# Performance work log

Hardware: AMD Instinct MI355X
Metric: run time of the kernel (lower is better)

## Reference

```python
import jax, jax.numpy as jnp
import numpy as np

N_WINDOW = 128  # |i-j| < N_WINDOW kept
D_K = 64

def setup_inputs() -> dict:
    key = jax.random.key(0)
    kq, kk, kv = jax.random.split(key, 3)
    B, H, S, D = 2, 8, 2048, D_K
    Q = jax.random.normal(kq, (B, H, S, D), dtype=jnp.float32)
    K = jax.random.normal(kk, (B, H, S, D), dtype=jnp.float32)
    V = jax.random.normal(kv, (B, H, S, D), dtype=jnp.float32)
    return {"Q": Q, "K": K, "V": V}

def reference(Q, K, V):
    S = Q.shape[-2]
    # scores: [B, H, S, S]
    scores = jnp.einsum('bhqd,bhkd->bhqk', Q, K) / jnp.sqrt(jnp.float32(D_K))
    idx = jnp.arange(S)
    band = jnp.abs(idx[:, None] - idx[None, :]) < N_WINDOW  # [S, S] band mask
    scores = jnp.where(band[None, None, :, :], scores, -jnp.inf)
    attn = jax.nn.softmax(scores, axis=-1)
    context = jnp.einsum('bhqk,bhkd->bhqd', attn, V)
    return (context, attn)
```

## Files before the change

### kernel.cpp

```cpp
#include <hip/hip_runtime.h>
#include <math.h>

#define S_LEN 2048
#define DK 64
#define NW 128
#define TQ 32
#define CH 32
#define NCH 10
#define KLW 320
#define PSTR 324
#define PSTR4 81
#define SSTR 68
#define SSTR4 17

#define DOT4(acc, a, b) \
    acc.x = fmaf(a.x, b.x, acc.x); \
    acc.y = fmaf(a.y, b.y, acc.y); \
    acc.z = fmaf(a.z, b.z, acc.z); \
    acc.w = fmaf(a.w, b.w, acc.w);

#define AXPY4(acc, s, v) \
    acc.x = fmaf(s, v.x, acc.x); \
    acc.y = fmaf(s, v.y, acc.y); \
    acc.z = fmaf(s, v.z, acc.z); \
    acc.w = fmaf(s, v.w, acc.w);

__global__ __launch_bounds__(256, 2) void band_attn_tile(
    const float* __restrict__ Q,
    const float* __restrict__ K,
    const float* __restrict__ V,
    float* __restrict__ ctx_out,
    float* __restrict__ attn_out)
{
    __shared__ float Qs[TQ * SSTR];
    __shared__ float St[CH * SSTR];
    __shared__ float Ps[TQ * PSTR];

    const int tid  = threadIdx.x;
    const int bh   = blockIdx.x >> 6;
    const int q0   = (blockIdx.x & 63) * TQ;
    const int base = q0 - (NW - 1);

    float4* Qs4 = (float4*)Qs;
    float4* St4 = (float4*)St;
    float4* Ps4 = (float4*)Ps;

    {
        const float4* Q4 = (const float4*)(Q + ((size_t)bh * S_LEN + q0) * DK);
        #pragma unroll
        for (int h = 0; h < 2; ++h) {
            int idx = tid + h * 256;
            int r = idx >> 4, c4 = idx & 15;
            float4 v = Q4[r * 16 + c4];
            v.x *= 0.125f; v.y *= 0.125f; v.z *= 0.125f; v.w *= 0.125f;
            Qs4[r * SSTR4 + c4] = v;
        }
    }

    const int q2 = tid >> 4;
    const int kb = tid & 15;
    const int qA = 2 * q2, qB = qA + 1;

    const float4* Kh4 = (const float4*)(K + (size_t)bh * S_LEN * DK);
    const float4* Vh4 = (const float4*)(V + (size_t)bh * S_LEN * DK);

    for (int c = 0; c < NCH; ++c) {
        __syncthreads();
        #pragma unroll
        for (int h = 0; h < 2; ++h) {
            int idx = tid + h * 256;
            int r = idx >> 4, c4 = idx & 15;
            int kg = base + c * CH + r;
            float4 v = {0.f, 0.f, 0.f, 0.f};
            if (kg >= 0 && kg < S_LEN) v = Kh4[(size_t)kg * 16 + c4];
            St4[r * SSTR4 + c4] = v;
        }
        __syncthreads();

        float4 a00 = {0,0,0,0}, a01 = {0,0,0,0}, a10 = {0,0,0,0}, a11 = {0,0,0,0};
        #pragma unroll
        for (int j = 0; j < 16; ++j) {
            float4 qa = Qs4[qA * SSTR4 + j];
            float4 qb = Qs4[qB * SSTR4 + j];
            float4 k0 = St4[kb * SSTR4 + j];
            float4 k1 = St4[(kb + 16) * SSTR4 + j];
            DOT4(a00, qa, k0); DOT4(a01, qa, k1);
            DOT4(a10, qb, k0); DOT4(a11, qb, k1);
        }
        float s00 = (a00.x + a00.y) + (a00.z + a00.w);
        float s01 = (a01.x + a01.y) + (a01.z + a01.w);
        float s10 = (a10.x + a10.y) + (a10.z + a10.w);
        float s11 = (a11.x + a11.y) + (a11.z + a11.w);

        const int klA = c * CH + kb, klB = klA + 16;
        const int kgA = base + klA, kgB = base + klB;
        const bool okA = (kgA >= 0) && (kgA < S_LEN);
        const bool okB = (kgB >= 0) && (kgB < S_LEN);
        Ps[qA * PSTR + klA] = (okA && klA >= qA && klA <= qA + 254) ? s00 : -INFINITY;
        Ps[qA * PSTR + klB] = (okB && klB >= qA && klB <= qA + 254) ? s01 : -INFINITY;
        Ps[qB * PSTR + klA] = (okA && klA >= qB && klA <= qB + 254) ? s10 : -INFINITY;
        Ps[qB * PSTR + klB] = (okB && klB >= qB && klB <= qB + 254) ? s11 : -INFINITY;
    }
    __syncthreads();

    {
        const int wv = tid >> 6, ln = tid & 63;
        for (int rr = 0; rr < 8; ++rr) {
            const int r = wv * 8 + rr;
            float v[5];
            #pragma unroll
            for (int j = 0; j < 5; ++j) v[j] = Ps[r * PSTR + ln + 64 * j];
            float m = v[0];
            #pragma unroll
            for (int j = 1; j < 5; ++j) m = fmaxf(m, v[j]);
            #pragma unroll
            for (int off = 32; off > 0; off >>= 1) m = fmaxf(m, __shfl_xor(m, off, 64));
            float e[5], sum = 0.f;
            #pragma unroll
            for (int j = 0; j < 5; ++j) { e[j] = __expf(v[j] - m); sum += e[j]; }
            #pragma unroll
            for (int off = 32; off > 0; off >>= 1) sum += __shfl_xor(sum, off, 64);
            const float inv = 1.0f / sum;
            #pragma unroll
            for (int j = 0; j < 5; ++j) Ps[r * PSTR + ln + 64 * j] = e[j] * inv;
        }
    }

    const int qp = tid >> 4;
    const int dq = tid & 15;
    const int cqA = 2 * qp, cqB = cqA + 1;
    float4 accA = {0,0,0,0}, accB = {0,0,0,0};
    for (int c = 0; c < NCH; ++c) {
        __syncthreads();
        #pragma unroll
        for (int h = 0; h < 2; ++h) {
            int idx = tid + h * 256;
            int r = idx >> 4, c4 = idx & 15;
            int kg = base + c * CH + r;
            float4 v = {0.f, 0.f, 0.f, 0.f};
            if (kg >= 0 && kg < S_LEN) v = Vh4[(size_t)kg * 16 + c4];
            St4[r * SSTR4 + c4] = v;
        }
        __syncthreads();
        #pragma unroll
        for (int t0 = 0; t0 < CH; t0 += 4) {
            const int idx4 = c * 8 + (t0 >> 2);
            float4 pA = Ps4[cqA * PSTR4 + idx4];
            float4 pB = Ps4[cqB * PSTR4 + idx4];
            float4 v0 = St4[(t0 + 0) * SSTR4 + dq];
            float4 v1 = St4[(t0 + 1) * SSTR4 + dq];
            float4 v2 = St4[(t0 + 2) * SSTR4 + dq];
            float4 v3 = St4[(t0 + 3) * SSTR4 + dq];
            AXPY4(accA, pA.x, v0); AXPY4(accA, pA.y, v1);
            AXPY4(accA, pA.z, v2); AXPY4(accA, pA.w, v3);
            AXPY4(accB, pB.x, v0); AXPY4(accB, pB.y, v1);
            AXPY4(accB, pB.z, v2); AXPY4(accB, pB.w, v3);
        }
    }

    {
        float4* C4 = (float4*)(ctx_out + (size_t)bh * S_LEN * DK);
        C4[(size_t)(q0 + cqA) * 16 + dq] = accA;
        C4[(size_t)(q0 + cqB) * 16 + dq] = accB;
    }

    {
        float4* A4 = (float4*)(attn_out + ((size_t)bh * S_LEN + q0) * S_LEN);
        for (int r = 0; r < TQ; ++r) {
            float4* row4 = A4 + (size_t)r * (S_LEN / 4);
            #pragma unroll
            for (int h = 0; h < 2; ++h) {
                const int idx = tid + h * 256;
                const int b0 = idx * 4 - base;
                float4 v = {0.f, 0.f, 0.f, 0.f};
                if (b0 + 3 >= 0 && b0 < KLW) {
                    const float* pr = Ps + r * PSTR;
                    v.x = ((unsigned)(b0 + 0) < KLW) ? pr[b0 + 0] : 0.f;
                    v.y = ((unsigned)(b0 + 1) < KLW) ? pr[b0 + 1] : 0.f;
                    v.z = ((unsigned)(b0 + 2) < KLW) ? pr[b0 + 2] : 0.f;
                    v.w = ((unsigned)(b0 + 3) < KLW) ? pr[b0 + 3] : 0.f;
                }
                row4[idx] = v;
            }
        }
    }
}

extern "C" void kernel_launch(void* const* d_in, const int* in_sizes, int n_in,
                              void* d_out, int out_size, void* d_ws, size_t ws_size,
                              hipStream_t stream) {
    const float* Q = (const float*)d_in[0];
    const float* K = (const float*)d_in[1];
    const float* V = (const float*)d_in[2];
    float* out = (float*)d_out;

    const int BH = in_sizes[0] / (S_LEN * DK);
    const size_t ctx_elems = (size_t)BH * S_LEN * DK;
    float* ctx  = out;
    float* attn = out + ctx_elems;

    dim3 grid(BH * (S_LEN / TQ));
    band_attn_tile<<<grid, 256, 0, stream>>>(Q, K, V, ctx, attn);
}
```

Measured before the change: 353.0 us.

## Use bf16 MFMA for QK and PV in band attention tile kernel

Replaces the scalar FP32 dot-product and AXPY loops with bf16 MFMA 16x16x32 instructions for both the score and context matmuls, converting Q, K, V and probabilities to bf16 in shared memory. Chunk size doubles to 64 keys and the key window base is aligned so the attention-row store reads whole float4s from shared memory. This targets ALU and LDS instruction cost, at the expense of reduced precision and a transposed scalar V store into LDS that may cause bank conflicts.

```diff
diff --git a/kernel.cpp b/kernel.cpp
--- a/kernel.cpp
+++ b/kernel.cpp
@@ -3,185 +3,175 @@
 
 #define S_LEN 2048
 #define DK 64
-#define NW 128
 #define TQ 32
-#define CH 32
-#define NCH 10
 #define KLW 320
+#define CH 64
+#define NCH 5
 #define PSTR 324
 #define PSTR4 81
-#define SSTR 68
-#define SSTR4 17
+#define KSTR 72
+#define KSTR4 18
 
-#define DOT4(acc, a, b) \
-    acc.x = fmaf(a.x, b.x, acc.x); \
-    acc.y = fmaf(a.y, b.y, acc.y); \
-    acc.z = fmaf(a.z, b.z, acc.z); \
-    acc.w = fmaf(a.w, b.w, acc.w);
+typedef __attribute__((ext_vector_type(8))) short bf16x8;
+typedef __attribute__((ext_vector_type(4))) float f32x4;
+typedef __attribute__((ext_vector_type(4))) short short4v;
 
-#define AXPY4(acc, s, v) \
-    acc.x = fmaf(s, v.x, acc.x); \
-    acc.y = fmaf(s, v.y, acc.y); \
-    acc.z = fmaf(s, v.z, acc.z); \
-    acc.w = fmaf(s, v.w, acc.w);
+__device__ __forceinline__ short f2bf(float f) {
+    unsigned u = __float_as_uint(f);
+    unsigned r = (u + 0x7fffu + ((u >> 16) & 1u)) >> 16;
+    return (short)r;
+}
 
-__global__ __launch_bounds__(256, 2) void band_attn_tile(
+__global__ __launch_bounds__(256, 2) void band_attn_mfma(
     const float* __restrict__ Q,
     const float* __restrict__ K,
     const float* __restrict__ V,
     float* __restrict__ ctx_out,
     float* __restrict__ attn_out)
 {
-    __shared__ float Qs[TQ * SSTR];
-    __shared__ float St[CH * SSTR];
-    __shared__ float Ps[TQ * PSTR];
+    __shared__ __align__(16) float Ps[TQ * PSTR];
+    __shared__ __align__(16) short Qs[TQ * KSTR];
+    __shared__ __align__(16) short St[CH * KSTR];
 
     const int tid  = threadIdx.x;
     const int bh   = blockIdx.x >> 6;
     const int q0   = (blockIdx.x & 63) * TQ;
-    const int base = q0 - (NW - 1);
+    const int base = q0 - 128;
 
-    float4* Qs4 = (float4*)Qs;
-    float4* St4 = (float4*)St;
-    float4* Ps4 = (float4*)Ps;
+    const int lane = tid & 63;
+    const int wv   = tid >> 6;
+    const int col  = lane & 15;
+    const int quad = lane >> 4;
+
+    const float4* Qg = (const float4*)(Q + ((size_t)bh * S_LEN + q0) * DK);
+    const float4* Kg = (const float4*)(K + (size_t)bh * S_LEN * DK);
+    const float4* Vg = (const float4*)(V + (size_t)bh * S_LEN * DK);
 
     {
-        const float4* Q4 = (const float4*)(Q + ((size_t)bh * S_LEN + q0) * DK);
+        short4v* Qs4 = (short4v*)Qs;
         #pragma unroll
         for (int h = 0; h < 2; ++h) {
             int idx = tid + h * 256;
             int r = idx >> 4, c4 = idx & 15;
-            float4 v = Q4[r * 16 + c4];
-            v.x *= 0.125f; v.y *= 0.125f; v.z *= 0.125f; v.w *= 0.125f;
-            Qs4[r * SSTR4 + c4] = v;
+            float4 v = Qg[r * 16 + c4];
+            short4v s = { f2bf(v.x * 0.125f), f2bf(v.y * 0.125f),
+                          f2bf(v.z * 0.125f), f2bf(v.w * 0.125f) };
+            Qs4[r * KSTR4 + c4] = s;
         }
     }
 
-    const int q2 = tid >> 4;
-    const int kb = tid & 15;
-    const int qA = 2 * q2, qB = qA + 1;
-
-    const float4* Kh4 = (const float4*)(K + (size_t)bh * S_LEN * DK);
-    const float4* Vh4 = (const float4*)(V + (size_t)bh * S_LEN * DK);
-
     for (int c = 0; c < NCH; ++c) {
         __syncthreads();
-        #pragma unroll
-        for (int h = 0; h < 2; ++h) {
-            int idx = tid + h * 256;
-            int r = idx >> 4, c4 = idx & 15;
-            int kg = base + c * CH + r;
-            float4 v = {0.f, 0.f, 0.f, 0.f};
-            if (kg >= 0 && kg < S_LEN) v = Kh4[(size_t)kg * 16 + c4];
-            St4[r * SSTR4 + c4] = v;
+        {
+            short4v* St4 = (short4v*)St;
+            #pragma unroll
+            for (int h = 0; h < 4; ++h) {
+                int idx = tid + h * 256;
+                int r = idx >> 4, c4 = idx & 15;
+                int kg = base + c * CH + r;
+                float4 v = {0.f, 0.f, 0.f, 0.f};
+                if ((unsigned)kg < S_LEN) v = Kg[(size_t)kg * 16 + c4];
+                short4v s = { f2bf(v.x), f2bf(v.y), f2bf(v.z), f2bf(v.w) };
+                St4[r * KSTR4 + c4] = s;
+            }
         }
         __syncthreads();
 
-        float4 a00 = {0,0,0,0}, a01 = {0,0,0,0}, a10 = {0,0,0,0}, a11 = {0,0,0,0};
+        const int kl = c * CH + 16 * wv + col;
+        const int kg = base + kl;
         #pragma unroll
-        for (int j = 0; j < 16; ++j) {
-            float4 qa = Qs4[qA * SSTR4 + j];
-            float4 qb = Qs4[qB * SSTR4 + j];
-            float4 k0 = St4[kb * SSTR4 + j];
-            float4 k1 = St4[(kb + 16) * SSTR4 + j];
-            DOT4(a00, qa, k0); DOT4(a01, qa, k1);
-            DOT4(a10, qb, k0); DOT4(a11, qb, k1);
+        for (int qt = 0; qt < 2; ++qt) {
+            f32x4 acc = {0.f, 0.f, 0.f, 0.f};
+            #pragma unroll
+            for (int h = 0; h < 2; ++h) {
+                bf16x8 a = *(const bf16x8*)(Qs + (16 * qt + col) * KSTR + h * 32 + quad * 8);
+                bf16x8 b = *(const bf16x8*)(St + (16 * wv + col) * KSTR + h * 32 + quad * 8);
+                acc = __builtin_amdgcn_mfma_f32_16x16x32_bf16(a, b, acc, 0, 0, 0);
+            }
+            #pragma unroll
+            for (int r = 0; r < 4; ++r) {
+                int qloc = 16 * qt + quad * 4 + r;
+                bool ok = ((unsigned)kg < S_LEN) && (kl > qloc) && (kl <= qloc + 255);
+                Ps[qloc * PSTR + kl] = ok ? acc[r] : -INFINITY;
+            }
         }
-        float s00 = (a00.x + a00.y) + (a00.z + a00.w);
-        float s01 = (a01.x + a01.y) + (a01.z + a01.w);
-        float s10 = (a10.x + a10.y) + (a10.z + a10.w);
-        float s11 = (a11.x + a11.y) + (a11.z + a11.w);
-
-        const int klA = c * CH + kb, klB = klA + 16;
-        const int kgA = base + klA, kgB = base + klB;
-        const bool okA = (kgA >= 0) && (kgA < S_LEN);
-        const bool okB = (kgB >= 0) && (kgB < S_LEN);
-        Ps[qA * PSTR + klA] = (okA && klA >= qA && klA <= qA + 254) ? s00 : -INFINITY;
-        Ps[qA * PSTR + klB] = (okB && klB >= qA && klB <= qA + 254) ? s01 : -INFINITY;
-        Ps[qB * PSTR + klA] = (okA && klA >= qB && klA <= qB + 254) ? s10 : -INFINITY;
-        Ps[qB * PSTR + klB] = (okB && klB >= qB && klB <= qB + 254) ? s11 : -INFINITY;
     }
     __syncthreads();
 
-    {
-        const int wv = tid >> 6, ln = tid & 63;
-        for (int rr = 0; rr < 8; ++rr) {
-            const int r = wv * 8 + rr;
-            float v[5];
-            #pragma unroll
-            for (int j = 0; j < 5; ++j) v[j] = Ps[r * PSTR + ln + 64 * j];
-            float m = v[0];
-            #pragma unroll
-            for (int j = 1; j < 5; ++j) m = fmaxf(m, v[j]);
-            #pragma unroll
-            for (int off = 32; off > 0; off >>= 1) m = fmaxf(m, __shfl_xor(m, off, 64));
-            float e[5], sum = 0.f;
-            #pragma unroll
-            for (int j = 0; j < 5; ++j) { e[j] = __expf(v[j] - m); sum += e[j]; }
-            #pragma unroll
-            for (int off = 32; off > 0; off >>= 1) sum += __shfl_xor(sum, off, 64);
-            const float inv = 1.0f / sum;
-            #pragma unroll
-            for (int j = 0; j < 5; ++j) Ps[r * PSTR + ln + 64 * j] = e[j] * inv;
-        }
+    #pragma unroll
+    for (int rr = 0; rr < 8; ++rr) {
+        float* row = Ps + (wv * 8 + rr) * PSTR;
+        float v[5];
+        #pragma unroll
+        for (int j = 0; j < 5; ++j) v[j] = row[lane + 64 * j];
+        float m = fmaxf(fmaxf(fmaxf(v[0], v[1]), fmaxf(v[2], v[3])), v[4]);
+        #pragma unroll
+        for (int off = 32; off > 0; off >>= 1) m = fmaxf(m, __shfl_xor(m, off, 64));
+        float e[5], sum = 0.f;
+        #pragma unroll
+        for (int j = 0; j < 5; ++j) { e[j] = __expf(v[j] - m); sum += e[j]; }
+        #pragma unroll
+        for (int off = 32; off > 0; off >>= 1) sum += __shfl_xor(sum, off, 64);
+        const float inv = 1.0f / sum;
+        #pragma unroll
+        for (int j = 0; j < 5; ++j) row[lane + 64 * j] = e[j] * inv;
     }
 
-    const int qp = tid >> 4;
-    const int dq = tid & 15;
-    const int cqA = 2 * qp, cqB = cqA + 1;
-    float4 accA = {0,0,0,0}, accB = {0,0,0,0};
+    f32x4 o0 = {0.f, 0.f, 0.f, 0.f}, o1 = {0.f, 0.f, 0.f, 0.f};
     for (int c = 0; c < NCH; ++c) {
         __syncthreads();
+        {
+            #pragma unroll
+            for (int h = 0; h < 4; ++h) {
+                int idx = tid + h * 256;
+                int r = idx >> 4, c4 = idx & 15;
+                int kg = base + c * CH + r;
+                float4 v = {0.f, 0.f, 0.f, 0.f};
+                if ((unsigned)kg < S_LEN) v = Vg[(size_t)kg * 16 + c4];
+                St[(4 * c4 + 0) * KSTR + r] = f2bf(v.x);
+                St[(4 * c4 + 1) * KSTR + r] = f2bf(v.y);
+                St[(4 * c4 + 2) * KSTR + r] = f2bf(v.z);
+                St[(4 * c4 + 3) * KSTR + r] = f2bf(v.w);
+            }
+        }
+        __syncthreads();
+
         #pragma unroll
         for (int h = 0; h < 2; ++h) {
-            int idx = tid + h * 256;
-            int r = idx >> 4, c4 = idx & 15;
-            int kg = base + c * CH + r;
-            float4 v = {0.f, 0.f, 0.f, 0.f};
-            if (kg >= 0 && kg < S_LEN) v = Vh4[(size_t)kg * 16 + c4];
-            St4[r * SSTR4 + c4] = v;
-        }
-        __syncthreads();
-        #pragma unroll
-        for (int t0 = 0; t0 < CH; t0 += 4) {
-            const int idx4 = c * 8 + (t0 >> 2);
-            float4 pA = Ps4[cqA * PSTR4 + idx4];
-            float4 pB = Ps4[cqB * PSTR4 + idx4];
-            float4 v0 = St4[(t0 + 0) * SSTR4 + dq];
-            float4 v1 = St4[(t0 + 1) * SSTR4 + dq];
-            float4 v2 = St4[(t0 + 2) * SSTR4 + dq];
-            float4 v3 = St4[(t0 + 3) * SSTR4 + dq];
-            AXPY4(accA, pA.x, v0); AXPY4(accA, pA.y, v1);
-            AXPY4(accA, pA.z, v2); AXPY4(accA, pA.w, v3);
-            AXPY4(accB, pB.x, v0); AXPY4(accB, pB.y, v1);
-            AXPY4(accB, pB.z, v2); AXPY4(accB, pB.w, v3);
+            bf16x8 b = *(const bf16x8*)(St + (16 * wv + col) * KSTR + h * 32 + quad * 8);
+            #pragma unroll
+            for (int qt = 0; qt < 2; ++qt) {
+                const float* pp = Ps + (16 * qt + col) * PSTR + c * CH + h * 32 + quad * 8;
+                f32x4 p0 = *(const f32x4*)(pp);
+                f32x4 p1 = *(const f32x4*)(pp + 4);
+                bf16x8 a = { f2bf(p0[0]), f2bf(p0[1]), f2bf(p0[2]), f2bf(p0[3]),
+                             f2bf(p1[0]), f2bf(p1[1]), f2bf(p1[2]), f2bf(p1[3]) };
+                if (qt == 0) o0 = __builtin_amdgcn_mfma_f32_16x16x32_bf16(a, b, o0, 0, 0, 0);
+                else         o1 = __builtin_amdgcn_mfma_f32_16x16x32_bf16(a, b, o1, 0, 0, 0);
+            }
         }
     }
 
     {
-        float4* C4 = (float4*)(ctx_out + (size_t)bh * S_LEN * DK);
-        C4[(size_t)(q0 + cqA) * 16 + dq] = accA;
-        C4[(size_t)(q0 + cqB) * 16 + dq] = accB;
+        float* Cg = ctx_out + ((size_t)bh * S_LEN + q0) * DK;
+        #pragma unroll
+        for (int r = 0; r < 4; ++r) {
+            Cg[(size_t)(quad * 4 + r) * DK + 16 * wv + col]        = o0[r];
+            Cg[(size_t)(16 + quad * 4 + r) * DK + 16 * wv + col]   = o1[r];
+        }
     }
 
     {
-        float4* A4 = (float4*)(attn_out + ((size_t)bh * S_LEN + q0) * S_LEN);
+        f32x4* A4 = (f32x4*)(attn_out + ((size_t)bh * S_LEN + q0) * S_LEN);
+        const f32x4* Ps4 = (const f32x4*)Ps;
+        const int b0 = 4 * tid - base;
+        const int b1 = b0 + 1024;
+        const f32x4 z = {0.f, 0.f, 0.f, 0.f};
         for (int r = 0; r < TQ; ++r) {
-            float4* row4 = A4 + (size_t)r * (S_LEN / 4);
-            #pragma unroll
-            for (int h = 0; h < 2; ++h) {
-                const int idx = tid + h * 256;
-                const int b0 = idx * 4 - base;
-                float4 v = {0.f, 0.f, 0.f, 0.f};
-                if (b0 + 3 >= 0 && b0 < KLW) {
-                    const float* pr = Ps + r * PSTR;
-                    v.x = ((unsigned)(b0 + 0) < KLW) ? pr[b0 + 0] : 0.f;
-                    v.y = ((unsigned)(b0 + 1) < KLW) ? pr[b0 + 1] : 0.f;
-                    v.z = ((unsigned)(b0 + 2) < KLW) ? pr[b0 + 2] : 0.f;
-                    v.w = ((unsigned)(b0 + 3) < KLW) ? pr[b0 + 3] : 0.f;
-                }
-                row4[idx] = v;
-            }
+            f32x4 va = ((unsigned)b0 < KLW) ? Ps4[r * PSTR4 + (b0 >> 2)] : z;
+            f32x4 vb = ((unsigned)b1 < KLW) ? Ps4[r * PSTR4 + (b1 >> 2)] : z;
+            A4[(size_t)r * 512 + tid]       = va;
+            A4[(size_t)r * 512 + tid + 256] = vb;
         }
     }
 }
@@ -200,5 +190,5 @@
     float* attn = out + ctx_elems;
 
     dim3 grid(BH * (S_LEN / TQ));
-    band_attn_tile<<<grid, 256, 0, stream>>>(Q, K, V, ctx, attn);
+    band_attn_mfma<<<grid, 256, 0, stream>>>(Q, K, V, ctx, attn);
 }
```

Result: faster. 326.4 us (-7.5%).
